# Optimization experiments

Measured on AMD Instinct MI355X. Metric: run time of the kernel, lower is better.

Reference implementation:

```python
import jax, jax.numpy as jnp
import numpy as np

N, F_IN, HID, HEADS, NEA, E, G = 50000, 32, 64, 2, 2, 800000, 50
SLOPE = 0.2  # leaky_relu negative_slope


def setup_inputs() -> dict:
    key = jax.random.key(0)
    ks = jax.random.split(key, 24)
    x = jax.random.normal(ks[0], (N, F_IN), jnp.float32)
    src = jax.random.randint(ks[1], (E,), 0, N, jnp.int32)
    off = jax.random.randint(ks[2], (E,), 1, N, jnp.int32)
    dst = ((src + off) % N).astype(jnp.int32)  # guaranteed no self loops
    edge_index = jnp.stack([src, dst])
    edge_attr = jax.random.uniform(ks[3], (E, NEA), jnp.float32, 0.5, 3.0)  # distances (reciprocal taken in fwd)
    batch = (jnp.arange(N) // (N // G)).astype(jnp.int32)
    interface_pos = jnp.arange(0, N, 5, dtype=jnp.int32)  # 200 interface nodes/graph

    def glorot(k, shape, fan_in, fan_out):
        s = jnp.sqrt(6.0 / (fan_in + fan_out))
        return jax.random.uniform(k, shape, jnp.float32, -s, s)

    HC = HEADS * HID
    W0 = glorot(ks[4], (F_IN, HC), F_IN, HC)
    attl0 = glorot(ks[5], (HEADS, HID), HID, HID)
    attr0 = glorot(ks[6], (HEADS, HID), HID, HID)
    W12 = glorot(ks[7], (2, HID, HC), HID, HC)
    attl12 = glorot(ks[8], (2, HEADS, HID), HID, HID)
    attr12 = glorot(ks[9], (2, HEADS, HID), HID, HID)
    eW = glorot(ks[10], (3, NEA, HC), NEA, HC)
    eb = jnp.zeros((3, HC), jnp.float32)
    bconv = jnp.zeros((3, HID), jnp.float32)
    gate_w = glorot(ks[11], (HID, 1), HID, 1)
    gate_b = jnp.zeros((1,), jnp.float32)
    lin1_w = glorot(ks[12], (4 * HID, 2 * HID), 4 * HID, 2 * HID)
    lin1_b = jnp.zeros((2 * HID,), jnp.float32)
    lin2_w = glorot(ks[13], (2 * HID, 1), 2 * HID, 1)
    lin2_b = jnp.zeros((1,), jnp.float32)
    return dict(x=x, edge_index=edge_index, edge_attr=edge_attr, batch=batch,
                interface_pos=interface_pos, graph_num=G,
                W0=W0, attl0=attl0, attr0=attr0, W12=W12, attl12=attl12, attr12=attr12,
                eW=eW, eb=eb, bconv=bconv, gate_w=gate_w, gate_b=gate_b,
                lin1_w=lin1_w, lin1_b=lin1_b, lin2_w=lin2_w, lin2_b=lin2_b)


def segment_softmax(e, seg, n):
    m = jax.ops.segment_max(e, seg, num_segments=n)
    ex = jnp.exp(e - m[seg])
    d = jax.ops.segment_sum(ex, seg, num_segments=n)
    return ex / (d[seg] + 1e-16)


def gate_conv(h, W, att_l, att_r, eW, eb, b, src, dst, ea):
    # GATEConv, concat=False, dropout in eval mode (identity)
    n = h.shape[0]
    H, C = att_l.shape
    xl = (h @ W).reshape(n, H, C)                      # lin_l == lin_r
    al = (xl * att_l).sum(-1)                          # [N,H]
    ar = (xl * att_r).sum(-1)
    e = jax.nn.leaky_relu(al[src] + ar[dst], SLOPE)    # [E+N,H]
    alpha = segment_softmax(e, dst, n)
    ee = (ea @ eW + eb).reshape(-1, H, C)              # edge embeddings
    msg = (xl[src] + ee) * alpha[..., None]
    out = jax.ops.segment_sum(msg, dst, num_segments=n)
    return out.mean(1) + b                             # mean over heads + bias


def reference(x, edge_index, edge_attr, batch, interface_pos, graph_num,
              W0, attl0, attr0, W12, attl12, attr12, eW, eb, bconv,
              gate_w, gate_b, lin1_w, lin1_b, lin2_w, lin2_b):
    n = x.shape[0]
    ar_n = jnp.arange(n, dtype=edge_index.dtype)
    src = jnp.concatenate([edge_index[0], ar_n])       # add self loops
    dst = jnp.concatenate([edge_index[1], ar_n])
    ea = jnp.concatenate([1.0 / edge_attr,
                          jnp.zeros((n, edge_attr.shape[1]), edge_attr.dtype)], 0)

    h = jnp.tanh(gate_conv(x, W0, attl0, attr0, eW[0], eb[0], bconv[0], src, dst, ea))
    xmax = h
    for l in range(2):  # num_layers - 1 structurally distinct weight slices
        h = jnp.tanh(gate_conv(h, W12[l], attl12[l], attr12[l],
                               eW[l + 1], eb[l + 1], bconv[l + 1], src, dst, ea))
        xmax = jnp.maximum(xmax, h)                    # JumpingKnowledge('max')

    xi = xmax[interface_pos]                           # [Ni, hidden]
    bi = batch[interface_pos]
    add = jax.ops.segment_sum(xi, bi, num_segments=graph_num)
    cnt = jax.ops.segment_sum(jnp.ones((xi.shape[0],), xi.dtype), bi, num_segments=graph_num)
    mean = add / jnp.maximum(cnt, 1.0)[:, None]
    gate = (xi @ gate_w + gate_b)[:, 0]                # global self-attention gate
    a = segment_softmax(gate, bi, graph_num)
    attp = jax.ops.segment_sum(a[:, None] * xi, bi, num_segments=graph_num)
    mx = jax.ops.segment_max(xi, bi, num_segments=graph_num)
    pooled = jnp.concatenate([add, mean, attp, mx], -1)  # [G, 4*hidden]
    z = jnp.tanh(pooled @ lin1_w + lin1_b)             # dropout eval = identity
    return z @ lin2_w + lin2_b                         # [G, 1]
```

## Files before the change

kernel.cpp:

```cpp
#include <hip/hip_runtime.h>
#include <hip/hip_bf16.h>
#include <hip/hip_fp16.h>
#include <math.h>

#define N_NODES 50000
#define FIN     32
#define HID     64
#define HC      128
#define NE      800000
#define NET     850000
#define NI      10000
#define NG      50
#define PB      8

typedef _Float16 half8 __attribute__((ext_vector_type(8)));
typedef float float4v __attribute__((ext_vector_type(4)));

__device__ __forceinline__ float lrelu(float x) { return fmaxf(x, 0.2f * x); }

__device__ __forceinline__ unsigned fenc(float f) {
  unsigned u = __float_as_uint(f);
  return (u & 0x80000000u) ? ~u : (u | 0x80000000u);
}
__device__ __forceinline__ float fdec(unsigned u) {
  return (u & 0x80000000u) ? __uint_as_float(u ^ 0x80000000u) : __uint_as_float(~u);
}

__device__ __forceinline__ float rlf(float v, int l) {
  return __int_as_float(__builtin_amdgcn_readlane(__float_as_int(v), l));
}
__device__ __forceinline__ int rli(int v, int l) {
  return __builtin_amdgcn_readlane(v, l);
}

__global__ void k_histrank(const int* __restrict__ ei, int* __restrict__ deg,
                           int* __restrict__ rank) {
  int e = blockIdx.x * blockDim.x + threadIdx.x;
  if (e >= NET) return;
  int d = (e < NE) ? ei[NE + e] : (e - NE);
  rank[e] = atomicAdd(&deg[d], 1);
}

__global__ void k_base(const int* __restrict__ deg, int* __restrict__ start,
                       int* __restrict__ gcur) {
  __shared__ int buf[256];
  __shared__ int basesh;
  int t = threadIdx.x;
  int i = blockIdx.x * 256 + t;
  int v = (i < N_NODES) ? deg[i] : 0;
  buf[t] = v; __syncthreads();
  for (int off = 1; off < 256; off <<= 1) {
    int a = (t >= off) ? buf[t - off] : 0;
    __syncthreads();
    buf[t] += a;
    __syncthreads();
  }
  if (t == 255) basesh = atomicAdd(gcur, buf[255]);
  __syncthreads();
  if (i < N_NODES) start[i] = basesh + buf[t] - v;
}

__global__ void k_scatter(const int* __restrict__ ei, const float* __restrict__ eattr,
                          const int* __restrict__ start, const int* __restrict__ rank,
                          int2* __restrict__ erec) {
  int e = blockIdx.x * blockDim.x + threadIdx.x;
  if (e >= NET) return;
  int s, d; float ex, ey;
  if (e < NE) {
    s = ei[e]; d = ei[NE + e];
    float2 ea = ((const float2*)eattr)[e];
    ex = 1.0f / ea.x; ey = 1.0f / ea.y;
  } else {
    s = d = e - NE; ex = 0.f; ey = 0.f;
  }
  int pos = start[d] + rank[e];
  __half2 ea2 = __floats2half2_rn(ex, ey);
  erec[pos] = make_int2(s << 8, *(int*)&ea2);
}

template <int F>
__global__ __launch_bounds__(256) void k_linear_mfma(
    const float* __restrict__ h, const float* __restrict__ W,
    const float* __restrict__ attl, const float* __restrict__ attr,
    __half2* __restrict__ xl2h, float* __restrict__ al, float* __restrict__ ar) {
  __shared__ _Float16 hA[16 * F];
  __shared__ _Float16 hC[16 * 128];
  __shared__ float redl[16 * 4], redr[16 * 4];
  const int w = threadIdx.x >> 6, lane = threadIdx.x & 63;
  const int m = lane & 15, q = lane >> 4;
  const int n0 = blockIdx.x * 16;

  for (int i = threadIdx.x; i < 16 * F; i += 256)
    hA[i] = (_Float16)h[(size_t)n0 * F + i];
  __syncthreads();

  half8 a0, a1;
#pragma unroll
  for (int j = 0; j < 8; j++) a0[j] = hA[m * F + q * 8 + j];
  if constexpr (F == 64) {
#pragma unroll
    for (int j = 0; j < 8; j++) a1[j] = hA[m * F + 32 + q * 8 + j];
  }

  const int c0 = w * 32;
  float4v acc[2];
  float pl[4] = {0.f, 0.f, 0.f, 0.f}, pr[4] = {0.f, 0.f, 0.f, 0.f};
#pragma unroll
  for (int t = 0; t < 2; t++) {
    const int colg = c0 + t * 16 + m;
    half8 b0;
#pragma unroll
    for (int j = 0; j < 8; j++) b0[j] = (_Float16)W[(q * 8 + j) * HC + colg];
    float4v z = {0.f, 0.f, 0.f, 0.f};
    acc[t] = __builtin_amdgcn_mfma_f32_16x16x32_f16(a0, b0, z, 0, 0, 0);
    if constexpr (F == 64) {
      half8 b1;
#pragma unroll
      for (int j = 0; j < 8; j++) b1[j] = (_Float16)W[(32 + q * 8 + j) * HC + colg];
      acc[t] = __builtin_amdgcn_mfma_f32_16x16x32_f16(a1, b1, acc[t], 0, 0, 0);
    }
    const float atl = attl[colg], atr = attr[colg];
#pragma unroll
    for (int reg = 0; reg < 4; reg++) {
      float val = acc[t][reg];
      hC[(q * 4 + reg) * 128 + colg] = (_Float16)val;
      pl[reg] += val * atl;
      pr[reg] += val * atr;
    }
  }
#pragma unroll
  for (int off = 1; off < 16; off <<= 1) {
#pragma unroll
    for (int reg = 0; reg < 4; reg++) {
      pl[reg] += __shfl_xor(pl[reg], off, 64);
      pr[reg] += __shfl_xor(pr[reg], off, 64);
    }
  }
  if (m == 0) {
#pragma unroll
    for (int reg = 0; reg < 4; reg++) {
      redl[(q * 4 + reg) * 4 + w] = pl[reg];
      redr[(q * 4 + reg) * 4 + w] = pr[reg];
    }
  }
  __syncthreads();
  if (threadIdx.x < 32) {
    int node = threadIdx.x >> 1, head = threadIdx.x & 1;
    al[(n0 + node) * 2 + head] = redl[node * 4 + head * 2] + redl[node * 4 + head * 2 + 1];
    ar[(n0 + node) * 2 + head] = redr[node * 4 + head * 2] + redr[node * 4 + head * 2 + 1];
  }
  for (int i = threadIdx.x; i < 16 * 64; i += 256) {
    int node = i >> 6, cc = i & 63;
    xl2h[(size_t)(n0 + node) * HID + cc] =
        __halves2half2(hC[node * 128 + cc], hC[node * 128 + 64 + cc]);
  }
}

__global__ void k_aggregate(const __half2* __restrict__ xl2h, const float* __restrict__ alp,
                            const float2* __restrict__ ar2, const int* __restrict__ start,
                            const int* __restrict__ degarr, const int2* __restrict__ erec,
                            const float* __restrict__ eW2, const float* __restrict__ eb1,
                            const float* __restrict__ bconv1, float* __restrict__ hout) {
  const int gid = blockIdx.x * 4 + (threadIdx.x >> 6);
  if (gid >= N_NODES) return;
  const int lane = threadIdx.x & 63;
  const int lane4 = lane << 2;
  const int o0 = start[gid];
  const int deg = degarr[gid];
  const float2 arv = ar2[gid];
  const char* xbase = (const char*)xl2h;
  const char* albase = (const char*)alp;

  float accA0 = 0.f, accA1 = 0.f, accB0 = 0.f, accB1 = 0.f;
  float ld0 = 0.f, ld1 = 0.f, lex0 = 0.f, ley0 = 0.f, lex1 = 0.f, ley1 = 0.f;
  for (int base = 0; base < deg; base += 64) {
    int j = base + lane;
    int soff = 0; float p0 = 0.f, p1 = 0.f;
    if (j < deg) {
      int2 r = erec[o0 + j];
      soff = r.x;
      float2 eaf = __half22float2(*(__half2*)&r.y);
      float2 alv = *(const float2*)(albase + (soff >> 5));
      p0 = __expf(lrelu(alv.x + arv.x));
      p1 = __expf(lrelu(alv.y + arv.y));
      ld0 += p0; ld1 += p1;
      lex0 += p0 * eaf.x; ley0 += p0 * eaf.y;
      lex1 += p1 * eaf.x; ley1 += p1 * eaf.y;
    }
    int slen = min(64, deg - base);
    int j2 = 0;
    for (; j2 + 8 <= slen; j2 += 8) {
      float2 x0 = __half22float2(*(const __half2*)(xbase + rli(soff, j2)     + lane4));
      float2 x1 = __half22float2(*(const __half2*)(xbase + rli(soff, j2 + 1) + lane4));
      float2 x2 = __half22float2(*(const __half2*)(xbase + rli(soff, j2 + 2) + lane4));
      float2 x3 = __half22float2(*(const __half2*)(xbase + rli(soff, j2 + 3) + lane4));
      float2 x4 = __half22float2(*(const __half2*)(xbase + rli(soff, j2 + 4) + lane4));
      float2 x5 = __half22float2(*(const __half2*)(xbase + rli(soff, j2 + 5) + lane4));
      float2 x6 = __half22float2(*(const __half2*)(xbase + rli(soff, j2 + 6) + lane4));
      float2 x7 = __half22float2(*(const __half2*)(xbase + rli(soff, j2 + 7) + lane4));
      accA0 += rlf(p0, j2)     * x0.x; accA1 += rlf(p1, j2)     * x0.y;
      accB0 += rlf(p0, j2 + 1) * x1.x; accB1 += rlf(p1, j2 + 1) * x1.y;
      accA0 += rlf(p0, j2 + 2) * x2.x; accA1 += rlf(p1, j2 + 2) * x2.y;
      accB0 += rlf(p0, j2 + 3) * x3.x; accB1 += rlf(p1, j2 + 3) * x3.y;
      accA0 += rlf(p0, j2 + 4) * x4.x; accA1 += rlf(p1, j2 + 4) * x4.y;
      accB0 += rlf(p0, j2 + 5) * x5.x; accB1 += rlf(p1, j2 + 5) * x5.y;
      accA0 += rlf(p0, j2 + 6) * x6.x; accA1 += rlf(p1, j2 + 6) * x6.y;
      accB0 += rlf(p0, j2 + 7) * x7.x; accB1 += rlf(p1, j2 + 7) * x7.y;
    }
    for (; j2 + 4 <= slen; j2 += 4) {
      float2 x0 = __half22float2(*(const __half2*)(xbase + rli(soff, j2)     + lane4));
      float2 x1 = __half22float2(*(const __half2*)(xbase + rli(soff, j2 + 1) + lane4));
      float2 x2 = __half22float2(*(const __half2*)(xbase + rli(soff, j2 + 2) + lane4));
      float2 x3 = __half22float2(*(const __half2*)(xbase + rli(soff, j2 + 3) + lane4));
      accA0 += rlf(p0, j2)     * x0.x; accA1 += rlf(p1, j2)     * x0.y;
      accB0 += rlf(p0, j2 + 1) * x1.x; accB1 += rlf(p1, j2 + 1) * x1.y;
      accA0 += rlf(p0, j2 + 2) * x2.x; accA1 += rlf(p1, j2 + 2) * x2.y;
      accB0 += rlf(p0, j2 + 3) * x3.x; accB1 += rlf(p1, j2 + 3) * x3.y;
    }
    for (; j2 < slen; j2++) {
      float2 x0 = __half22float2(*(const __half2*)(xbase + rli(soff, j2) + lane4));
      accA0 += rlf(p0, j2) * x0.x; accA1 += rlf(p1, j2) * x0.y;
    }
  }
  float acc0 = accA0 + accB0, acc1 = accA1 + accB1;
#pragma unroll
  for (int off = 32; off; off >>= 1) {
    ld0  += __shfl_xor(ld0, off, 64);
    ld1  += __shfl_xor(ld1, off, 64);
    lex0 += __shfl_xor(lex0, off, 64);
    ley0 += __shfl_xor(ley0, off, 64);
    lex1 += __shfl_xor(lex1, off, 64);
    ley1 += __shfl_xor(ley1, off, 64);
  }
  float t0 = acc0 + eW2[lane]      * lex0 + eW2[HC + lane]      * ley0 + eb1[lane]      * ld0;
  float t1 = acc1 + eW2[64 + lane] * lex1 + eW2[HC + 64 + lane] * ley1 + eb1[64 + lane] * ld1;
  float r = 0.5f * (t0 / (ld0 + 1e-16f) + t1 / (ld1 + 1e-16f)) + bconv1[lane];
  hout[(size_t)gid * HID + lane] = tanhf(r);
}

__global__ void k_ranges(const int* __restrict__ ipos, const int* __restrict__ batch,
                         int* __restrict__ gstart) {
  int i = blockIdx.x * blockDim.x + threadIdx.x;
  if (i >= NI) return;
  int bi = batch[ipos[i]];
  int prev = (i > 0) ? batch[ipos[i - 1]] : -1;
  for (int g = prev + 1; g <= bi; g++) gstart[g] = i;
  if (i == NI - 1)
    for (int g = bi + 1; g <= NG; g++) gstart[g] = NI;
}

__global__ void k_pool(const float* __restrict__ h0, const float* __restrict__ h1,
                       const float* __restrict__ h2, const int* __restrict__ ipos,
                       const int* __restrict__ gstart, const float* __restrict__ gate_w,
                       const float* __restrict__ gate_b, float* __restrict__ add,
                       unsigned* __restrict__ mxE, float* __restrict__ cnt,
                       float* __restrict__ attp, float* __restrict__ aden) {
  __shared__ float red[4][3 * HID + 2];
  const int g = blockIdx.x / PB, m = blockIdx.x % PB;
  const int w = threadIdx.x >> 6, lane = threadIdx.x & 63;
  const int s0 = gstart[g], s1 = gstart[g + 1];
  const int len = s1 - s0;
  const int b0 = s0 + (len * m) / PB;
  const int b1 = s0 + (len * (m + 1)) / PB;
  const float gwv = gate_w[lane];
  const float gbv = gate_b[0];

  float padd = 0.f, pmax = -1e30f, pattp = 0.f, paden = 0.f, pcnt = 0.f;
  for (int i = b0 + w; i < b1; i += 4) {
    size_t node = (size_t)ipos[i] * HID + lane;
    float v = fmaxf(fmaxf(h0[node], h1[node]), h2[node]);
    padd += v;
    pmax = fmaxf(pmax, v);
    float gv = v * gwv;
#pragma unroll
    for (int off = 32; off; off >>= 1) gv += __shfl_xor(gv, off, 64);
    float e = __expf(gv + gbv);
    pattp += e * v;
    paden += e;
    pcnt += 1.f;
  }
  red[w][lane] = padd;
  red[w][HID + lane] = pmax;
  red[w][2 * HID + lane] = pattp;
  if (lane == 0) { red[w][3 * HID] = paden; red[w][3 * HID + 1] = pcnt; }
  __syncthreads();
  if (w == 0) {
    float addv  = red[0][lane] + red[1][lane] + red[2][lane] + red[3][lane];
    float maxv  = fmaxf(fmaxf(red[0][HID + lane], red[1][HID + lane]),
                        fmaxf(red[2][HID + lane], red[3][HID + lane]));
    float attpv = red[0][2 * HID + lane] + red[1][2 * HID + lane] +
                  red[2][2 * HID + lane] + red[3][2 * HID + lane];
    atomicAdd(&add[g * HID + lane], addv);
    atomicMax(&mxE[g * HID + lane], fenc(maxv));
    atomicAdd(&attp[g * HID + lane], attpv);
    if (lane == 0) {
      atomicAdd(&aden[g], red[0][3 * HID] + red[1][3 * HID] + red[2][3 * HID] + red[3][3 * HID]);
      atomicAdd(&cnt[g],  red[0][3 * HID + 1] + red[1][3 * HID + 1] +
                          red[2][3 * HID + 1] + red[3][3 * HID + 1]);
    }
  }
}

__global__ void k_final(const float* __restrict__ add, const float* __restrict__ cnt,
                        const float* __restrict__ attp, const float* __restrict__ aden,
                        const unsigned* __restrict__ mxE, const float* __restrict__ lin1_w,
                        const float* __restrict__ lin1_b, const float* __restrict__ lin2_w,
                        const float* __restrict__ lin2_b, float* __restrict__ out) {
  __shared__ float pooled[4 * HID];
  __shared__ float zred[2 * HID];
  int g = blockIdx.x, t = threadIdx.x;
  if (t < HID)            pooled[t] = add[g * HID + t];
  else if (t < 2 * HID)   pooled[t] = add[g * HID + (t - HID)] / fmaxf(cnt[g], 1.f);
  else if (t < 3 * HID)   pooled[t] = attp[g * HID + (t - 2 * HID)] / (aden[g] + 1e-16f);
  else                    pooled[t] = fdec(mxE[g * HID + (t - 3 * HID)]);
  __syncthreads();
  if (t < 2 * HID) {
    float z = lin1_b[t];
    for (int k = 0; k < 4 * HID; k++) z += pooled[k] * lin1_w[k * (2 * HID) + t];
    z = tanhf(z);
    zred[t] = z * lin2_w[t];
  }
  __syncthreads();
  if (t == 0) {
    float s = 0.f;
    for (int k = 0; k < 2 * HID; k++) s += zred[k];
    out[g] = s + lin2_b[0];
  }
}

extern "C" void kernel_launch(void* const* d_in, const int* in_sizes, int n_in,
                              void* d_out, int out_size, void* d_ws, size_t ws_size,
                              hipStream_t stream) {
  const float* x      = (const float*)d_in[0];
  const int*   ei     = (const int*)d_in[1];
  const float* eattr  = (const float*)d_in[2];
  const int*   batch  = (const int*)d_in[3];
  const int*   ipos   = (const int*)d_in[4];
  const float* W0     = (const float*)d_in[6];
  const float* attl0  = (const float*)d_in[7];
  const float* attr0  = (const float*)d_in[8];
  const float* W12    = (const float*)d_in[9];
  const float* attl12 = (const float*)d_in[10];
  const float* attr12 = (const float*)d_in[11];
  const float* eW     = (const float*)d_in[12];
  const float* eb     = (const float*)d_in[13];
  const float* bconv  = (const float*)d_in[14];
  const float* gate_w = (const float*)d_in[15];
  const float* gate_b = (const float*)d_in[16];
  const float* lin1_w = (const float*)d_in[17];
  const float* lin1_b = (const float*)d_in[18];
  const float* lin2_w = (const float*)d_in[19];
  const float* lin2_b = (const float*)d_in[20];
  float* out = (float*)d_out;

  char* ws = (char*)d_ws;
  size_t off = 0;
  auto alloc = [&](size_t elems) {
    void* p = ws + off;
    off += ((elems * 4 + 15) / 16) * 16;
    return p;
  };
  int*      deg    = (int*)alloc(N_NODES);
  int*      gcur   = (int*)alloc(4);
  float*    addp   = (float*)alloc(NG * HID);
  float*    attp   = (float*)alloc(NG * HID);
  unsigned* mxE    = (unsigned*)alloc(NG * HID);
  float*    cnt    = (float*)alloc(64);
  float*    aden   = (float*)alloc(64);
  size_t zbytes = off;
  int*     gstart = (int*)alloc(NG + 4);
  int*     start  = (int*)alloc(N_NODES);
  int*     rank   = (int*)alloc(NET);
  int2*    erec   = (int2*)alloc((size_t)NET * 2);
  __half2* xl2h   = (__half2*)alloc((size_t)N_NODES * HID);
  float*   al     = (float*)alloc((size_t)N_NODES * 2);
  float*   arr    = (float*)alloc((size_t)N_NODES * 2);
  float*   h0     = (float*)alloc((size_t)N_NODES * HID);
  float*   h1     = (float*)alloc((size_t)N_NODES * HID);
  float*   h2     = (float*)alloc((size_t)N_NODES * HID);
  (void)ws_size; (void)in_sizes; (void)n_in; (void)out_size;

  hipMemsetAsync(d_ws, 0, zbytes, stream);
  k_histrank<<<(NET + 255) / 256, 256, 0, stream>>>(ei, deg, rank);
  k_base<<<(N_NODES + 255) / 256, 256, 0, stream>>>(deg, start, gcur);
  k_scatter<<<(NET + 255) / 256, 256, 0, stream>>>(ei, eattr, start, rank, erec);
  k_ranges<<<(NI + 255) / 256, 256, 0, stream>>>(ipos, batch, gstart);

  k_linear_mfma<FIN><<<N_NODES / 16, 256, 0, stream>>>(x, W0, attl0, attr0, xl2h, al, arr);
  k_aggregate<<<N_NODES / 4, 256, 0, stream>>>(xl2h, al, (const float2*)arr,
                                               start, deg, erec, eW, eb, bconv, h0);
  k_linear_mfma<HID><<<N_NODES / 16, 256, 0, stream>>>(h0, W12, attl12, attr12, xl2h, al, arr);
  k_aggregate<<<N_NODES / 4, 256, 0, stream>>>(xl2h, al, (const float2*)arr,
                                               start, deg, erec, eW + 2 * HC, eb + HC,
                                               bconv + HID, h1);
  k_linear_mfma<HID><<<N_NODES / 16, 256, 0, stream>>>(h1, W12 + (size_t)HID * HC,
                                                       attl12 + HC, attr12 + HC, xl2h, al, arr);
  k_aggregate<<<N_NODES / 4, 256, 0, stream>>>(xl2h, al, (const float2*)arr,
                                               start, deg, erec, eW + 4 * HC, eb + 2 * HC,
                                               bconv + 2 * HID, h2);

  k_pool<<<NG * PB, 256, 0, stream>>>(h0, h1, h2, ipos, gstart, gate_w, gate_b,
                                      addp, mxE, cnt, attp, aden);
  k_final<<<NG, 256, 0, stream>>>(addp, cnt, attp, aden, mxE, lin1_w, lin1_b, lin2_w, lin2_b, out);
}
```

Before: 342.2 us.

## Aggregate two nodes per wavefront and fuse range kernel into histogram launch

The aggregation kernel now handles two destination nodes per 64-lane wavefront. Each half-wave loads up to 32 incoming edge records for its own node, and the gather loop interleaves feature loads for both nodes, so a wave keeps twice as many independent loads in flight. With an average degree around 17, this targets lanes that sat idle when one node filled a whole wave. The separate interface-range kernel is also folded into extra blocks of the histogram launch, removing one launch. The cost is loop trip count set by the larger of the two degrees, plus extra shuffles in the epilogue.

```diff
diff --git a/kernel.cpp b/kernel.cpp
--- a/kernel.cpp
+++ b/kernel.cpp
@@ -13,6 +13,8 @@
 #define NG      50
 #define PB      8
 
+#define HBLK    ((NET + 255) / 256)
+
 typedef _Float16 half8 __attribute__((ext_vector_type(8)));
 typedef float float4v __attribute__((ext_vector_type(4)));
 
@@ -33,12 +35,24 @@
   return __builtin_amdgcn_readlane(v, l);
 }
 
-__global__ void k_histrank(const int* __restrict__ ei, int* __restrict__ deg,
-                           int* __restrict__ rank) {
-  int e = blockIdx.x * blockDim.x + threadIdx.x;
-  if (e >= NET) return;
-  int d = (e < NE) ? ei[NE + e] : (e - NE);
-  rank[e] = atomicAdd(&deg[d], 1);
+__global__ void k_hist_ranges(const int* __restrict__ ei, int* __restrict__ deg,
+                              int* __restrict__ rank, const int* __restrict__ ipos,
+                              const int* __restrict__ batch, int* __restrict__ gstart) {
+  int b = blockIdx.x;
+  if (b < HBLK) {
+    int e = b * 256 + threadIdx.x;
+    if (e >= NET) return;
+    int d = (e < NE) ? ei[NE + e] : (e - NE);
+    rank[e] = atomicAdd(&deg[d], 1);
+  } else {
+    int i = (b - HBLK) * 256 + threadIdx.x;
+    if (i >= NI) return;
+    int bi = batch[ipos[i]];
+    int prev = (i > 0) ? batch[ipos[i - 1]] : -1;
+    for (int g = prev + 1; g <= bi; g++) gstart[g] = i;
+    if (i == NI - 1)
+      for (int g = bi + 1; g <= NG; g++) gstart[g] = NI;
+  }
 }
 
 __global__ void k_base(const int* __restrict__ deg, int* __restrict__ start,
@@ -156,75 +170,78 @@
   }
 }
 
-__global__ void k_aggregate(const __half2* __restrict__ xl2h, const float* __restrict__ alp,
-                            const float2* __restrict__ ar2, const int* __restrict__ start,
-                            const int* __restrict__ degarr, const int2* __restrict__ erec,
-                            const float* __restrict__ eW2, const float* __restrict__ eb1,
-                            const float* __restrict__ bconv1, float* __restrict__ hout) {
-  const int gid = blockIdx.x * 4 + (threadIdx.x >> 6);
-  if (gid >= N_NODES) return;
+__global__ __launch_bounds__(256) void k_aggregate(
+    const __half2* __restrict__ xl2h, const float* __restrict__ alp,
+    const float2* __restrict__ ar2, const int* __restrict__ start,
+    const int* __restrict__ degarr, const int2* __restrict__ erec,
+    const float* __restrict__ eW2, const float* __restrict__ eb1,
+    const float* __restrict__ bconv1, float* __restrict__ hout) {
+  const int gid0 = blockIdx.x * 8 + (threadIdx.x >> 6) * 2;
   const int lane = threadIdx.x & 63;
+  const int l32 = lane & 31;
+  const int half = lane >> 5;
   const int lane4 = lane << 2;
-  const int o0 = start[gid];
-  const int deg = degarr[gid];
-  const float2 arv = ar2[gid];
+  const int gidH = gid0 + half;
+  const int o0H = start[gidH];
+  const int degH = degarr[gidH];
+  const float2 arvH = ar2[gidH];
   const char* xbase = (const char*)xl2h;
   const char* albase = (const char*)alp;
 
-  float accA0 = 0.f, accA1 = 0.f, accB0 = 0.f, accB1 = 0.f;
+  const int degA = rli(degH, 0);
+  const int degB = rli(degH, 32);
+  const int degmax = max(degA, degB);
+
+  float aA0 = 0.f, aA1 = 0.f, bA0 = 0.f, bA1 = 0.f;
+  float aB0 = 0.f, aB1 = 0.f, bB0 = 0.f, bB1 = 0.f;
   float ld0 = 0.f, ld1 = 0.f, lex0 = 0.f, ley0 = 0.f, lex1 = 0.f, ley1 = 0.f;
-  for (int base = 0; base < deg; base += 64) {
-    int j = base + lane;
+
+  for (int base = 0; base < degmax; base += 32) {
+    int j = base + l32;
     int soff = 0; float p0 = 0.f, p1 = 0.f;
-    if (j < deg) {
-      int2 r = erec[o0 + j];
+    if (j < degH) {
+      int2 r = erec[o0H + j];
       soff = r.x;
       float2 eaf = __half22float2(*(__half2*)&r.y);
       float2 alv = *(const float2*)(albase + (soff >> 5));
-      p0 = __expf(lrelu(alv.x + arv.x));
-      p1 = __expf(lrelu(alv.y + arv.y));
+      p0 = __expf(lrelu(alv.x + arvH.x));
+      p1 = __expf(lrelu(alv.y + arvH.y));
       ld0 += p0; ld1 += p1;
       lex0 += p0 * eaf.x; ley0 += p0 * eaf.y;
       lex1 += p1 * eaf.x; ley1 += p1 * eaf.y;
     }
-    int slen = min(64, deg - base);
-    int j2 = 0;
-    for (; j2 + 8 <= slen; j2 += 8) {
-      float2 x0 = __half22float2(*(const __half2*)(xbase + rli(soff, j2)     + lane4));
-      float2 x1 = __half22float2(*(const __half2*)(xbase + rli(soff, j2 + 1) + lane4));
-      float2 x2 = __half22float2(*(const __half2*)(xbase + rli(soff, j2 + 2) + lane4));
-      float2 x3 = __half22float2(*(const __half2*)(xbase + rli(soff, j2 + 3) + lane4));
-      float2 x4 = __half22float2(*(const __half2*)(xbase + rli(soff, j2 + 4) + lane4));
-      float2 x5 = __half22float2(*(const __half2*)(xbase + rli(soff, j2 + 5) + lane4));
-      float2 x6 = __half22float2(*(const __half2*)(xbase + rli(soff, j2 + 6) + lane4));
-      float2 x7 = __half22float2(*(const __half2*)(xbase + rli(soff, j2 + 7) + lane4));
-      accA0 += rlf(p0, j2)     * x0.x; accA1 += rlf(p1, j2)     * x0.y;
-      accB0 += rlf(p0, j2 + 1) * x1.x; accB1 += rlf(p1, j2 + 1) * x1.y;
-      accA0 += rlf(p0, j2 + 2) * x2.x; accA1 += rlf(p1, j2 + 2) * x2.y;
-      accB0 += rlf(p0, j2 + 3) * x3.x; accB1 += rlf(p1, j2 + 3) * x3.y;
-      accA0 += rlf(p0, j2 + 4) * x4.x; accA1 += rlf(p1, j2 + 4) * x4.y;
-      accB0 += rlf(p0, j2 + 5) * x5.x; accB1 += rlf(p1, j2 + 5) * x5.y;
-      accA0 += rlf(p0, j2 + 6) * x6.x; accA1 += rlf(p1, j2 + 6) * x6.y;
-      accB0 += rlf(p0, j2 + 7) * x7.x; accB1 += rlf(p1, j2 + 7) * x7.y;
-    }
-    for (; j2 + 4 <= slen; j2 += 4) {
-      float2 x0 = __half22float2(*(const __half2*)(xbase + rli(soff, j2)     + lane4));
-      float2 x1 = __half22float2(*(const __half2*)(xbase + rli(soff, j2 + 1) + lane4));
-      float2 x2 = __half22float2(*(const __half2*)(xbase + rli(soff, j2 + 2) + lane4));
-      float2 x3 = __half22float2(*(const __half2*)(xbase + rli(soff, j2 + 3) + lane4));
-      accA0 += rlf(p0, j2)     * x0.x; accA1 += rlf(p1, j2)     * x0.y;
-      accB0 += rlf(p0, j2 + 1) * x1.x; accB1 += rlf(p1, j2 + 1) * x1.y;
-      accA0 += rlf(p0, j2 + 2) * x2.x; accA1 += rlf(p1, j2 + 2) * x2.y;
-      accB0 += rlf(p0, j2 + 3) * x3.x; accB1 += rlf(p1, j2 + 3) * x3.y;
-    }
-    for (; j2 < slen; j2++) {
-      float2 x0 = __half22float2(*(const __half2*)(xbase + rli(soff, j2) + lane4));
-      accA0 += rlf(p0, j2) * x0.x; accA1 += rlf(p1, j2) * x0.y;
-    }
-  }
-  float acc0 = accA0 + accB0, acc1 = accA1 + accB1;
-#pragma unroll
-  for (int off = 32; off; off >>= 1) {
+    int lenA = min(32, degA - base); lenA = max(lenA, 0);
+    int lenB = min(32, degB - base); lenB = max(lenB, 0);
+    int lenA4 = (lenA + 3) & ~3;
+    int lenB4 = (lenB + 3) & ~3;
+    int len = max(lenA4, lenB4);
+    for (int j2 = 0; j2 < len; j2 += 4) {
+      if (j2 < lenA4) {
+        float2 x0 = __half22float2(*(const __half2*)(xbase + rli(soff, j2)     + lane4));
+        float2 x1 = __half22float2(*(const __half2*)(xbase + rli(soff, j2 + 1) + lane4));
+        float2 x2 = __half22float2(*(const __half2*)(xbase + rli(soff, j2 + 2) + lane4));
+        float2 x3 = __half22float2(*(const __half2*)(xbase + rli(soff, j2 + 3) + lane4));
+        aA0 += rlf(p0, j2)     * x0.x; aA1 += rlf(p1, j2)     * x0.y;
+        bA0 += rlf(p0, j2 + 1) * x1.x; bA1 += rlf(p1, j2 + 1) * x1.y;
+        aA0 += rlf(p0, j2 + 2) * x2.x; aA1 += rlf(p1, j2 + 2) * x2.y;
+        bA0 += rlf(p0, j2 + 3) * x3.x; bA1 += rlf(p1, j2 + 3) * x3.y;
+      }
+      if (j2 < lenB4) {
+        float2 x4 = __half22float2(*(const __half2*)(xbase + rli(soff, 32 + j2)     + lane4));
+        float2 x5 = __half22float2(*(const __half2*)(xbase + rli(soff, 32 + j2 + 1) + lane4));
+        float2 x6 = __half22float2(*(const __half2*)(xbase + rli(soff, 32 + j2 + 2) + lane4));
+        float2 x7 = __half22float2(*(const __half2*)(xbase + rli(soff, 32 + j2 + 3) + lane4));
+        aB0 += rlf(p0, 32 + j2)     * x4.x; aB1 += rlf(p1, 32 + j2)     * x4.y;
+        bB0 += rlf(p0, 32 + j2 + 1) * x5.x; bB1 += rlf(p1, 32 + j2 + 1) * x5.y;
+        aB0 += rlf(p0, 32 + j2 + 2) * x6.x; aB1 += rlf(p1, 32 + j2 + 2) * x6.y;
+        bB0 += rlf(p0, 32 + j2 + 3) * x7.x; bB1 += rlf(p1, 32 + j2 + 3) * x7.y;
+      }
+    }
+  }
+  float accA0 = aA0 + bA0, accA1 = aA1 + bA1;
+  float accB0 = aB0 + bB0, accB1 = aB1 + bB1;
+#pragma unroll
+  for (int off = 16; off; off >>= 1) {
     ld0  += __shfl_xor(ld0, off, 64);
     ld1  += __shfl_xor(ld1, off, 64);
     lex0 += __shfl_xor(lex0, off, 64);
@@ -232,21 +249,25 @@
     lex1 += __shfl_xor(lex1, off, 64);
     ley1 += __shfl_xor(ley1, off, 64);
   }
-  float t0 = acc0 + eW2[lane]      * lex0 + eW2[HC + lane]      * ley0 + eb1[lane]      * ld0;
-  float t1 = acc1 + eW2[64 + lane] * lex1 + eW2[HC + 64 + lane] * ley1 + eb1[64 + lane] * ld1;
-  float r = 0.5f * (t0 / (ld0 + 1e-16f) + t1 / (ld1 + 1e-16f)) + bconv1[lane];
-  hout[(size_t)gid * HID + lane] = tanhf(r);
-}
-
-__global__ void k_ranges(const int* __restrict__ ipos, const int* __restrict__ batch,
-                         int* __restrict__ gstart) {
-  int i = blockIdx.x * blockDim.x + threadIdx.x;
-  if (i >= NI) return;
-  int bi = batch[ipos[i]];
-  int prev = (i > 0) ? batch[ipos[i - 1]] : -1;
-  for (int g = prev + 1; g <= bi; g++) gstart[g] = i;
-  if (i == NI - 1)
-    for (int g = bi + 1; g <= NG; g++) gstart[g] = NI;
+  float ld0A  = __shfl(ld0,  l32, 64), ld0B  = __shfl(ld0,  32 + l32, 64);
+  float ld1A  = __shfl(ld1,  l32, 64), ld1B  = __shfl(ld1,  32 + l32, 64);
+  float lex0A = __shfl(lex0, l32, 64), lex0B = __shfl(lex0, 32 + l32, 64);
+  float ley0A = __shfl(ley0, l32, 64), ley0B = __shfl(ley0, 32 + l32, 64);
+  float lex1A = __shfl(lex1, l32, 64), lex1B = __shfl(lex1, 32 + l32, 64);
+  float ley1A = __shfl(ley1, l32, 64), ley1B = __shfl(ley1, 32 + l32, 64);
+
+  const float w00 = eW2[lane],      w01 = eW2[HC + lane],      b0v = eb1[lane];
+  const float w10 = eW2[64 + lane], w11 = eW2[HC + 64 + lane], b1v = eb1[64 + lane];
+  const float bc = bconv1[lane];
+
+  float tA0 = accA0 + w00 * lex0A + w01 * ley0A + b0v * ld0A;
+  float tA1 = accA1 + w10 * lex1A + w11 * ley1A + b1v * ld1A;
+  float tB0 = accB0 + w00 * lex0B + w01 * ley0B + b0v * ld0B;
+  float tB1 = accB1 + w10 * lex1B + w11 * ley1B + b1v * ld1B;
+  float rA = 0.5f * (tA0 / (ld0A + 1e-16f) + tA1 / (ld1A + 1e-16f)) + bc;
+  float rB = 0.5f * (tB0 / (ld0B + 1e-16f) + tB1 / (ld1B + 1e-16f)) + bc;
+  hout[(size_t)gid0 * HID + lane] = tanhf(rA);
+  hout[(size_t)(gid0 + 1) * HID + lane] = tanhf(rB);
 }
 
 __global__ void k_pool(const float* __restrict__ h0, const float* __restrict__ h1,
@@ -381,21 +402,20 @@
   (void)ws_size; (void)in_sizes; (void)n_in; (void)out_size;
 
   hipMemsetAsync(d_ws, 0, zbytes, stream);
-  k_histrank<<<(NET + 255) / 256, 256, 0, stream>>>(ei, deg, rank);
+  k_hist_ranges<<<HBLK + (NI + 255) / 256, 256, 0, stream>>>(ei, deg, rank, ipos, batch, gstart);
   k_base<<<(N_NODES + 255) / 256, 256, 0, stream>>>(deg, start, gcur);
   k_scatter<<<(NET + 255) / 256, 256, 0, stream>>>(ei, eattr, start, rank, erec);
-  k_ranges<<<(NI + 255) / 256, 256, 0, stream>>>(ipos, batch, gstart);
 
   k_linear_mfma<FIN><<<N_NODES / 16, 256, 0, stream>>>(x, W0, attl0, attr0, xl2h, al, arr);
-  k_aggregate<<<N_NODES / 4, 256, 0, stream>>>(xl2h, al, (const float2*)arr,
+  k_aggregate<<<N_NODES / 8, 256, 0, stream>>>(xl2h, al, (const float2*)arr,
                                                start, deg, erec, eW, eb, bconv, h0);
   k_linear_mfma<HID><<<N_NODES / 16, 256, 0, stream>>>(h0, W12, attl12, attr12, xl2h, al, arr);
-  k_aggregate<<<N_NODES / 4, 256, 0, stream>>>(xl2h, al, (const float2*)arr,
+  k_aggregate<<<N_NODES / 8, 256, 0, stream>>>(xl2h, al, (const float2*)arr,
                                                start, deg, erec, eW + 2 * HC, eb + HC,
                                                bconv + HID, h1);
   k_linear_mfma<HID><<<N_NODES / 16, 256, 0, stream>>>(h1, W12 + (size_t)HID * HC,
                                                        attl12 + HC, attr12 + HC, xl2h, al, arr);
-  k_aggregate<<<N_NODES / 4, 256, 0, stream>>>(xl2h, al, (const float2*)arr,
+  k_aggregate<<<N_NODES / 8, 256, 0, stream>>>(xl2h, al, (const float2*)arr,
                                                start, deg, erec, eW + 4 * HC, eb + 2 * HC,
                                                bconv + 2 * HID, h2);
 
```

Measured after the change: 344.3 us. Within noise of the previous version (+0.6%).
